# Kernel optimization log

Measured on AMD Instinct MI355X. Metric: run time of the kernel, lower is better.

## Reference

```python
import jax, jax.numpy as jnp
import numpy as np

N = 50000   # num_of_nodes (cfg.dataset.num_nodes)
C = 128     # in_channels; TopKPooling ratio = C/N -> k = C pooled nodes
E = 800000  # num edges


def setup_inputs() -> dict:
    key = jax.random.key(0)
    ks = jax.random.split(key, 8)
    std = 1.0 / np.sqrt(C)
    X = jax.random.normal(ks[0], (N, C), dtype=jnp.float32)
    edge_index = jax.random.randint(ks[1], (2, E), 0, N, dtype=jnp.int64)
    edge_weight = jax.random.uniform(ks[2], (E,), dtype=jnp.float32)
    p = jax.random.normal(ks[3], (C,), dtype=jnp.float32)                      # TopKPooling projection
    W_ih = jax.random.normal(ks[4], (3 * C, C), dtype=jnp.float32) * std       # GRU input weights [r|z|n]
    W_hh = jax.random.normal(ks[5], (3 * C, C), dtype=jnp.float32) * std       # GRU hidden weights
    b_ih = jnp.zeros((3 * C,), dtype=jnp.float32)
    b_hh = jnp.zeros((3 * C,), dtype=jnp.float32)
    W_conv = jax.random.uniform(ks[6], (C, C), dtype=jnp.float32, minval=-std, maxval=std)  # GCN lin weight
    b_conv = jnp.zeros((C,), dtype=jnp.float32)
    return {"X": X, "edge_weight": edge_weight, "p": p, "W_ih": W_ih, "W_hh": W_hh,
            "b_ih": b_ih, "b_hh": b_hh, "W_conv": W_conv, "b_conv": b_conv,
            "edge_index": edge_index}


def _forward(X, edge_weight, p, W_ih, W_hh, b_ih, b_hh, W_conv, b_conv, edge_index):
    # ---- TopKPooling: score = X.p/||p||, pick top k=C nodes, gate with tanh ----
    score = X @ p / jnp.linalg.norm(p)                       # [N]
    top_vals, top_idx = jax.lax.top_k(score, C)              # k = C (ratio = C/N)
    X_tilde = X[top_idx] * jnp.tanh(top_vals)[:, None]       # [C, C]
    X_tilde = jax.lax.stop_gradient(X_tilde)                 # .detach() in original

    # ---- GRU single step: input X_tilde (batch=C), hidden h0 = W_conv ----
    gi = X_tilde @ W_ih.T + b_ih                             # [C, 3C]
    gh = W_conv @ W_hh.T + b_hh                              # [C, 3C]
    gi_r, gi_z, gi_n = jnp.split(gi, 3, axis=-1)
    gh_r, gh_z, gh_n = jnp.split(gh, 3, axis=-1)
    r = jax.nn.sigmoid(gi_r + gh_r)
    z = jax.nn.sigmoid(gi_z + gh_z)
    n = jnp.tanh(gi_n + r * gh_n)
    W_new = (1.0 - z) * n + z * W_conv                       # evolved GCN weight [C, C]

    # ---- GCNConv with self-loops + symmetric normalization ----
    src, dst = edge_index[0], edge_index[1]
    loop = jnp.arange(N, dtype=src.dtype)
    src2 = jnp.concatenate([src, loop])
    dst2 = jnp.concatenate([dst, loop])
    w2 = jnp.concatenate([edge_weight, jnp.ones((N,), dtype=edge_weight.dtype)])
    deg = jax.ops.segment_sum(w2, dst2, num_segments=N)      # [N]
    dinv = jnp.where(deg > 0, jax.lax.rsqrt(deg), 0.0)
    norm = dinv[src2] * w2 * dinv[dst2]                      # [E+N]
    Xw = X @ W_new.T                                         # [N, C]
    msg = Xw[src2] * norm[:, None]                           # gather + scale, [E+N, C]
    out = jax.ops.segment_sum(msg, dst2, num_segments=N)     # scatter-add, [N, C]
    return out + b_conv


def reference(X, edge_weight, p, W_ih, W_hh, b_ih, b_hh, W_conv, b_conv, edge_index):
    return _forward(X, edge_weight, p, W_ih, W_hh, b_ih, b_hh, W_conv, b_conv, edge_index)
```

## Files before the change

kernel.cpp:

```cpp
#include <hip/hip_runtime.h>
#include <hip/hip_fp16.h>
#include <math.h>

#define C 128
#define HB 2048
#define NS 4096
#define SHB 192

typedef __attribute__((ext_vector_type(8))) short bf16x8;
typedef __attribute__((ext_vector_type(4))) float f32x4;

__device__ inline unsigned ord_f32(float f) {
    unsigned u = __float_as_uint(f);
    return u ^ ((u & 0x80000000u) ? 0xFFFFFFFFu : 0x80000000u);
}
__device__ inline float unord_f32(unsigned u) {
    return __uint_as_float(u ^ ((u & 0x80000000u) ? 0x80000000u : 0xFFFFFFFFu));
}
__device__ inline short f2bf(float f) {
    unsigned u = __float_as_uint(f);
    return (short)((u + 0x7FFFu + ((u >> 16) & 1u)) >> 16);
}
__device__ inline float bf2f(short s) {
    return __uint_as_float(((unsigned)(unsigned short)s) << 16);
}

__global__ __launch_bounds__(1024) void k_front(const float* __restrict__ X,
                                                const float* __restrict__ p,
                                                float* __restrict__ scores,
                                                int* __restrict__ hist,
                                                const int* __restrict__ ei,
                                                int* __restrict__ rh,
                                                int N, int E, int NBIN, int NBLKE) {
    int t = threadIdx.x;
    if (blockIdx.x < SHB) {
        __shared__ int lh[HB];
        for (int i = t; i < HB; i += 1024) lh[i] = 0;
        __syncthreads();
        int gw   = blockIdx.x * 16 + (t >> 6);
        int lane = t & 63;
        const float2* p2 = (const float2*)p;
        float2 pv2 = p2[lane];
        for (int r = gw; r < N; r += SHB * 16) {
            const float2* xr = (const float2*)(X + (size_t)r * C);
            float2 x2 = xr[lane];
            float a = x2.x * pv2.x + x2.y * pv2.y;
            #pragma unroll
            for (int o = 32; o; o >>= 1) a += __shfl_down(a, o);
            if (lane == 0) {
                scores[r] = a;
                atomicAdd(&lh[ord_f32(a) >> 21], 1);
            }
        }
        __syncthreads();
        for (int i = t; i < HB; i += 1024) {
            int v = lh[i];
            if (v) atomicAdd(&hist[i], v);
        }
    } else {
        __shared__ int bh[8][256];
        int cp = (t >> 7) & 7;
        for (int i = t; i < 8 * 256; i += 1024) ((int*)bh)[i] = 0;
        __syncthreads();
        int eb = blockIdx.x - SHB;
        int e = eb * 2048 + t * 2;
        if (e + 1 < E) {
            int2 d2 = *(const int2*)(ei + E + e);
            atomicAdd(&bh[cp][d2.x >> 8], 1);
            atomicAdd(&bh[cp][d2.y >> 8], 1);
        } else if (e < E) {
            atomicAdd(&bh[cp][ei[E + e] >> 8], 1);
        }
        __syncthreads();
        for (int i = t; i < NBIN; i += 1024) {
            int s = 0;
            #pragma unroll
            for (int c = 0; c < 8; c++) s += bh[c][i];
            rh[(size_t)i * NBLKE + eb] = s;
        }
    }
}

__global__ __launch_bounds__(512) void k_rscanA(int* __restrict__ rh, int* __restrict__ tot, int NBLKE) {
    __shared__ int sc[512];
    int t = threadIdx.x;
    int bin = blockIdx.x;
    int v = (t < NBLKE) ? rh[(size_t)bin * NBLKE + t] : 0;
    sc[t] = v;
    __syncthreads();
    for (int off = 1; off < 512; off <<= 1) {
        int u = (t >= off) ? sc[t - off] : 0;
        __syncthreads();
        sc[t] += u;
        __syncthreads();
    }
    if (t < NBLKE) rh[(size_t)bin * NBLKE + t] = sc[t] - v;
    if (t == 511) tot[bin] = sc[511];
}

__global__ __launch_bounds__(1024) void k_rscat(const int* __restrict__ ei, const float* __restrict__ ew,
                                                const int* __restrict__ rh, const int* __restrict__ tot,
                                                unsigned long long* __restrict__ sorted,
                                                int E, int NBIN, int NBLKE) {
    __shared__ int sc[256];
    __shared__ int cur[256];
    int t = threadIdx.x;
    int eb = blockIdx.x;
    int v = 0;
    if (t < 256) {
        v = (t < NBIN) ? tot[t] : 0;
        sc[t] = v;
    }
    __syncthreads();
    for (int off = 1; off < 256; off <<= 1) {
        int u = (t < 256 && t >= off) ? sc[t - off] : 0;
        __syncthreads();
        if (t < 256) sc[t] += u;
        __syncthreads();
    }
    if (t < NBIN) cur[t] = (sc[t] - v) + rh[(size_t)t * NBLKE + eb];
    __syncthreads();
    int e = eb * 2048 + t * 2;
    #pragma unroll
    for (int j = 0; j < 2; j++) {
        int ee = e + j;
        if (ee < E) {
            int s = ei[ee], d = ei[E + ee];
            float w = ew[ee];
            int pos = atomicAdd(&cur[d >> 8], 1);
            unsigned long long pk = ((unsigned long long)(unsigned)d << 48)
                                  | ((unsigned long long)(unsigned short)s << 32)
                                  |  (unsigned long long)__float_as_uint(w);
            sorted[pos] = pk;
        }
    }
}

__global__ __launch_bounds__(1024) void k_bin(const unsigned long long* __restrict__ sorted,
                                              const int* __restrict__ tot,
                                              int* __restrict__ offs, float* __restrict__ dinv,
                                              unsigned* __restrict__ epack,
                                              int N, int E, int NBIN) {
    __shared__ int cnt[256];
    __shared__ float wsum[256];
    __shared__ int sc[256];
    __shared__ int cur2[256];
    __shared__ int s_base[2];
    int t = threadIdx.x;
    int b = blockIdx.x;
    int v = 0;
    if (t < 256) {
        v = (t < NBIN) ? tot[t] : 0;
        sc[t] = v;
    }
    __syncthreads();
    for (int off = 1; off < 256; off <<= 1) {
        int u = (t < 256 && t >= off) ? sc[t - off] : 0;
        __syncthreads();
        if (t < 256) sc[t] += u;
        __syncthreads();
    }
    if (t == b) { s_base[0] = sc[t] - v; s_base[1] = sc[t]; }
    __syncthreads();
    int s0 = s_base[0], s1 = s_base[1];
    for (int i = t; i < 256; i += 1024) { cnt[i] = 0; wsum[i] = 0.f; }
    __syncthreads();
    for (int i = s0 + t; i < s1; i += 1024) {
        unsigned long long pk = sorted[i];
        int d8 = (int)(pk >> 48) & 255;
        float w = __uint_as_float((unsigned)(pk & 0xFFFFFFFFull));
        atomicAdd(&cnt[d8], 1);
        atomicAdd(&wsum[d8], w);
    }
    __syncthreads();
    int cv = (t < 256) ? cnt[t] : 0;
    if (t < 256) sc[t] = cv;
    __syncthreads();
    for (int off = 1; off < 256; off <<= 1) {
        int u = (t < 256 && t >= off) ? sc[t - off] : 0;
        __syncthreads();
        if (t < 256) sc[t] += u;
        __syncthreads();
    }
    if (t < 256) {
        int loff = sc[t] - cv;
        cur2[t] = s0 + loff;
        int node = b * 256 + t;
        if (node < N) {
            offs[node] = s0 + loff;
            dinv[node] = rsqrtf(1.0f + wsum[t]);
        }
    }
    if (b == NBIN - 1 && t == 0) offs[N] = E;
    __syncthreads();
    for (int i = s0 + t; i < s1; i += 1024) {
        unsigned long long pk = sorted[i];
        int d8 = (int)(pk >> 48) & 255;
        unsigned src = (unsigned)((pk >> 32) & 0xFFFFu);
        float w = __uint_as_float((unsigned)(pk & 0xFFFFFFFFull));
        int pos = atomicAdd(&cur2[d8], 1);
        __half hw = __float2half(w);
        epack[pos] = ((unsigned)*(unsigned short*)&hw << 16) | src;
    }
}

__global__ __launch_bounds__(256) void k_filter(const float* __restrict__ scores,
                                                const int* __restrict__ hist,
                                                int* __restrict__ nc,
                                                unsigned long long* __restrict__ cand, int N) {
    __shared__ int sc[256];
    __shared__ int sT;
    int t = threadIdx.x;
    int loc[8];
    int sum = 0;
    #pragma unroll
    for (int s = 0; s < 8; s++) {
        loc[s] = hist[HB - 1 - (t * 8 + s)];
        sum += loc[s];
    }
    sc[t] = sum;
    __syncthreads();
    for (int off = 1; off < 256; off <<= 1) {
        int v = (t >= off) ? sc[t - off] : 0;
        __syncthreads();
        sc[t] += v;
        __syncthreads();
    }
    int run = sc[t] - sum;
    #pragma unroll
    for (int s = 0; s < 8; s++) {
        int b = HB - 1 - (t * 8 + s);
        int nr = run + loc[s];
        if (run < C && nr >= C) sT = b;
        run = nr;
    }
    __syncthreads();
    int T = sT;
    int i = blockIdx.x * 256 + t;
    if (i < N) {
        unsigned u = ord_f32(scores[i]);
        if ((int)(u >> 21) >= T) {
            int pos = atomicAdd(nc, 1);
            if (pos < NS)
                cand[pos] = ((unsigned long long)u << 32) | (unsigned)(~(unsigned)i);
        }
    }
}

__global__ __launch_bounds__(1024) void k_sel(const unsigned long long* __restrict__ cand,
                                              const int* __restrict__ nc,
                                              const float* __restrict__ p,
                                              int* __restrict__ tidx, float* __restrict__ gate) {
    __shared__ unsigned long long sk[NS];
    __shared__ float red[16];
    __shared__ float s_pn;
    int t = threadIdx.x;
    int M = *nc; if (M > NS) M = NS;
    int S = 256; while (S < M) S <<= 1;
    for (int i = t; i < S; i += 1024) sk[i] = (i < M) ? cand[i] : 0ULL;
    float pv = 0.f;
    if (t < C) { float x = p[t]; pv = x * x; }
    #pragma unroll
    for (int o = 32; o; o >>= 1) pv += __shfl_down(pv, o);
    if ((t & 63) == 0) red[t >> 6] = pv;
    __syncthreads();
    if (t == 0) {
        float s = 0.f;
        for (int i = 0; i < 16; i++) s += red[i];
        s_pn = sqrtf(s);
    }
    for (int k = 2; k <= S; k <<= 1) {
        for (int j = k >> 1; j > 0; j >>= 1) {
            __syncthreads();
            for (int idx = t; idx < S; idx += 1024) {
                int l = idx ^ j;
                if (l > idx) {
                    unsigned long long a = sk[idx], b = sk[l];
                    bool desc = (idx & k) == 0;
                    if (desc ? (a < b) : (a > b)) { sk[idx] = b; sk[l] = a; }
                }
            }
        }
    }
    __syncthreads();
    if (t < C) {
        unsigned long long g = sk[t];
        tidx[t] = (int)(~(unsigned)(g & 0xFFFFFFFFull));
        gate[t] = tanhf(unord_f32((unsigned)(g >> 32)) / s_pn);
    }
}

__global__ __launch_bounds__(256) void k_gru(const float* __restrict__ X,
                                             const int* __restrict__ tidx,
                                             const float* __restrict__ gate,
                                             const float* __restrict__ Wc,
                                             const float* __restrict__ W_ih, const float* __restrict__ W_hh,
                                             const float* __restrict__ b_ih, const float* __restrict__ b_hh,
                                             float* __restrict__ wnewT) {
    int t = threadIdx.x;
    int i = t & 127;
    int j = blockIdx.x * 2 + (t >> 7);
    int src = tidx[i];
    float g = gate[i];
    const float4* xr   = (const float4*)(X + (size_t)src * C);
    const float4* hr   = (const float4*)(Wc + (size_t)i * C);
    const float4* wri  = (const float4*)(W_ih + (size_t)j * C);
    const float4* wzi  = (const float4*)(W_ih + (size_t)(C + j) * C);
    const float4* wni  = (const float4*)(W_ih + (size_t)(2 * C + j) * C);
    const float4* wrh  = (const float4*)(W_hh + (size_t)j * C);
    const float4* wzh  = (const float4*)(W_hh + (size_t)(C + j) * C);
    const float4* wnh  = (const float4*)(W_hh + (size_t)(2 * C + j) * C);
    float gir = 0, giz = 0, gin = 0, ghr = 0, ghz = 0, ghn = 0;
    #pragma unroll 8
    for (int k4 = 0; k4 < C / 4; k4++) {
        float4 x = xr[k4], h = hr[k4], a;
        a = wri[k4]; gir += x.x * a.x + x.y * a.y + x.z * a.z + x.w * a.w;
        a = wzi[k4]; giz += x.x * a.x + x.y * a.y + x.z * a.z + x.w * a.w;
        a = wni[k4]; gin += x.x * a.x + x.y * a.y + x.z * a.z + x.w * a.w;
        a = wrh[k4]; ghr += h.x * a.x + h.y * a.y + h.z * a.z + h.w * a.w;
        a = wzh[k4]; ghz += h.x * a.x + h.y * a.y + h.z * a.z + h.w * a.w;
        a = wnh[k4]; ghn += h.x * a.x + h.y * a.y + h.z * a.z + h.w * a.w;
    }
    gir = g * gir + b_ih[j];         ghr += b_hh[j];
    giz = g * giz + b_ih[C + j];     ghz += b_hh[C + j];
    gin = g * gin + b_ih[2 * C + j]; ghn += b_hh[2 * C + j];
    float r = 1.f / (1.f + expf(-(gir + ghr)));
    float z = 1.f / (1.f + expf(-(giz + ghz)));
    float n = tanhf(gin + r * ghn);
    float wn = (1.f - z) * n + z * Wc[(size_t)i * C + j];
    wnewT[(size_t)j * C + i] = wn;
}

__global__ __launch_bounds__(256) void k_xw(const float* __restrict__ X,
                                            const float* __restrict__ wnewT,
                                            const float* __restrict__ dinv,
                                            unsigned* __restrict__ xwh, int N) {
    __shared__ short Bh[C * C];
    __shared__ short Bl[C * C];
    int t = threadIdx.x;
    for (int idx = t; idx < C * C; idx += 256) {
        int k = idx >> 7, c = idx & 127;
        float wv = wnewT[idx];
        short hi = f2bf(wv);
        float lo = wv - bf2f(hi);
        int pos = c * C + (k ^ ((c & 15) << 3));
        Bh[pos] = hi;
        Bl[pos] = f2bf(lo);
    }
    __syncthreads();

    int wave = t >> 6, lane = t & 63;
    int ln = lane & 15, quad = lane >> 4;
    int r0 = blockIdx.x * 128 + wave * 32;

    f32x4 acc[2][8];
    #pragma unroll
    for (int mt = 0; mt < 2; mt++)
        #pragma unroll
        for (int ct = 0; ct < 8; ct++) { acc[mt][ct][0] = 0.f; acc[mt][ct][1] = 0.f; acc[mt][ct][2] = 0.f; acc[mt][ct][3] = 0.f; }

    int row0 = r0 + ln;       if (row0 >= N) row0 = N - 1;
    int row1 = r0 + 16 + ln;  if (row1 >= N) row1 = N - 1;
    const float* xr0 = X + (size_t)row0 * C + quad * 8;
    const float* xr1 = X + (size_t)row1 * C + quad * 8;

    for (int ks = 0; ks < 4; ks++) {
        float a0[8], a1[8];
        *(float4*)&a0[0] = *(const float4*)(xr0 + ks * 32);
        *(float4*)&a0[4] = *(const float4*)(xr0 + ks * 32 + 4);
        *(float4*)&a1[0] = *(const float4*)(xr1 + ks * 32);
        *(float4*)&a1[4] = *(const float4*)(xr1 + ks * 32 + 4);
        bf16x8 a0h, a0l, a1h, a1l;
        #pragma unroll
        for (int j = 0; j < 8; j++) {
            short h0 = f2bf(a0[j]); a0h[j] = h0; a0l[j] = f2bf(a0[j] - bf2f(h0));
            short h1 = f2bf(a1[j]); a1h[j] = h1; a1l[j] = f2bf(a1[j] - bf2f(h1));
        }
        int kb = ks * 32 + quad * 8;
        int koff = kb ^ (ln << 3);
        #pragma unroll
        for (int ct = 0; ct < 8; ct++) {
            int pos = (ct * 16 + ln) * C + koff;
            bf16x8 bh = *(bf16x8*)&Bh[pos];
            bf16x8 bl = *(bf16x8*)&Bl[pos];
            acc[0][ct] = __builtin_amdgcn_mfma_f32_16x16x32_bf16(a0h, bh, acc[0][ct], 0, 0, 0);
            acc[0][ct] = __builtin_amdgcn_mfma_f32_16x16x32_bf16(a0l, bh, acc[0][ct], 0, 0, 0);
            acc[0][ct] = __builtin_amdgcn_mfma_f32_16x16x32_bf16(a0h, bl, acc[0][ct], 0, 0, 0);
            acc[1][ct] = __builtin_amdgcn_mfma_f32_16x16x32_bf16(a1h, bh, acc[1][ct], 0, 0, 0);
            acc[1][ct] = __builtin_amdgcn_mfma_f32_16x16x32_bf16(a1l, bh, acc[1][ct], 0, 0, 0);
            acc[1][ct] = __builtin_amdgcn_mfma_f32_16x16x32_bf16(a1h, bl, acc[1][ct], 0, 0, 0);
        }
    }

    __half* H = (__half*)xwh;
    #pragma unroll
    for (int mt = 0; mt < 2; mt++) {
        int rbase = r0 + mt * 16 + quad * 4;
        #pragma unroll
        for (int reg = 0; reg < 4; reg++) {
            int r = rbase + reg;
            if (r < N) {
                float dvr = dinv[r];
                #pragma unroll
                for (int ct = 0; ct < 8; ct++) {
                    int col = ct * 16 + ln;
                    H[(size_t)r * C + col] = __float2half(acc[mt][ct][reg] * dvr);
                }
            }
        }
    }
}

__global__ __launch_bounds__(256) void k_gather(const unsigned* __restrict__ xwh,
                                                const int* __restrict__ offs,
                                                const unsigned* __restrict__ epack,
                                                const float* __restrict__ dinv,
                                                const float* __restrict__ b_conv,
                                                float* __restrict__ out, int N) {
    int t = threadIdx.x;
    int v = blockIdx.x * 4 + (t >> 6);
    int lane = t & 63;
    if (v >= N) return;
    float dv = dinv[v];
    unsigned uv = xwh[(size_t)v * 64 + lane];
    __half2 hv = *(__half2*)&uv;
    float acc0 = __low2float(hv);
    float acc1 = __high2float(hv);
    int e0 = offs[v], e1 = offs[v + 1];
    int e = e0;
    for (; e + 7 < e1; e += 8) {
        unsigned pk[8], ux[8];
        #pragma unroll
        for (int j = 0; j < 8; j++) pk[j] = __builtin_nontemporal_load(&epack[e + j]);
        #pragma unroll
        for (int j = 0; j < 8; j++) ux[j] = xwh[(size_t)(pk[j] & 0xFFFFu) * 64 + lane];
        #pragma unroll
        for (int j = 0; j < 8; j++) {
            unsigned short hs = (unsigned short)(pk[j] >> 16);
            float nm = __half2float(*(__half*)&hs);
            __half2 h = *(__half2*)&ux[j];
            acc0 += nm * __low2float(h);
            acc1 += nm * __high2float(h);
        }
    }
    for (; e + 3 < e1; e += 4) {
        unsigned pk[4], ux[4];
        #pragma unroll
        for (int j = 0; j < 4; j++) pk[j] = __builtin_nontemporal_load(&epack[e + j]);
        #pragma unroll
        for (int j = 0; j < 4; j++) ux[j] = xwh[(size_t)(pk[j] & 0xFFFFu) * 64 + lane];
        #pragma unroll
        for (int j = 0; j < 4; j++) {
            unsigned short hs = (unsigned short)(pk[j] >> 16);
            float nm = __half2float(*(__half*)&hs);
            __half2 h = *(__half2*)&ux[j];
            acc0 += nm * __low2float(h);
            acc1 += nm * __high2float(h);
        }
    }
    for (; e < e1; e++) {
        unsigned pA = __builtin_nontemporal_load(&epack[e]);
        unsigned uA = xwh[(size_t)(pA & 0xFFFFu) * 64 + lane];
        unsigned short hs = (unsigned short)(pA >> 16);
        float nA = __half2float(*(__half*)&hs);
        __half2 hA = *(__half2*)&uA;
        acc0 += nA * __low2float(hA);
        acc1 += nA * __high2float(hA);
    }
    const float2* b2 = (const float2*)b_conv;
    float2 bb = b2[lane];
    unsigned long long ov = ((unsigned long long)__float_as_uint(acc1 * dv + bb.y) << 32)
                          |  (unsigned long long)__float_as_uint(acc0 * dv + bb.x);
    __builtin_nontemporal_store(ov, (unsigned long long*)(out + (size_t)v * C) + lane);
}

extern "C" void kernel_launch(void* const* d_in, const int* in_sizes, int n_in,
                              void* d_out, int out_size, void* d_ws, size_t ws_size,
                              hipStream_t stream) {
    const float* X      = (const float*)d_in[0];
    const float* ew     = (const float*)d_in[1];
    const float* p      = (const float*)d_in[2];
    const float* W_ih   = (const float*)d_in[3];
    const float* W_hh   = (const float*)d_in[4];
    const float* b_ih   = (const float*)d_in[5];
    const float* b_hh   = (const float*)d_in[6];
    const float* W_conv = (const float*)d_in[7];
    const float* b_conv = (const float*)d_in[8];
    const int*   ei     = (const int*)d_in[9];
    const int N = in_sizes[0] / C;
    const int E = in_sizes[1];
    float* out = (float*)d_out;
    const int NB    = (N + 255) / 256;
    const int NBIN  = (N + 255) / 256;
    const int NBLKE = (E + 2047) / 2048;

    char* w = (char*)d_ws;
    auto alloc = [&](size_t bytes) -> void* {
        void* r = (void*)w;
        w += (bytes + 255) & ~(size_t)255;
        return r;
    };
    int*   hist   = (int*)alloc(HB * 4);
    int*   nc     = (int*)alloc(256);
    size_t zbytes = (size_t)(w - (char*)d_ws);
    float* scores = (float*)alloc((size_t)N * 4);
    float* dinv   = (float*)alloc((size_t)N * 4);
    int*   offs   = (int*)alloc((size_t)(N + 1) * 4);
    int*   rh     = (int*)alloc((size_t)NBIN * NBLKE * 4);
    int*   tot    = (int*)alloc((size_t)NBIN * 4);
    unsigned long long* cand = (unsigned long long*)alloc((size_t)NS * 8);
    int*   tidx   = (int*)alloc(C * 4);
    float* gate   = (float*)alloc(C * 4);
    float* wnewT  = (float*)alloc((size_t)C * C * 4);
    unsigned long long* sorted = (unsigned long long*)alloc((size_t)E * 8);
    unsigned* epack = (unsigned*)alloc((size_t)E * 4);
    unsigned* xwh = (unsigned*)alloc((size_t)N * 64 * 4);

    hipMemsetAsync(d_ws, 0, zbytes, stream);
    k_front<<<SHB + NBLKE, 1024, 0, stream>>>(X, p, scores, hist, ei, rh, N, E, NBIN, NBLKE);
    k_filter<<<NB, 256, 0, stream>>>(scores, hist, nc, cand, N);
    k_sel<<<1, 1024, 0, stream>>>(cand, nc, p, tidx, gate);
    k_gru<<<C / 2, 256, 0, stream>>>(X, tidx, gate, W_conv, W_ih, W_hh, b_ih, b_hh, wnewT);
    k_rscanA<<<NBIN, 512, 0, stream>>>(rh, tot, NBLKE);
    k_rscat<<<NBLKE, 1024, 0, stream>>>(ei, ew, rh, tot, sorted, E, NBIN, NBLKE);
    k_bin<<<NBIN, 1024, 0, stream>>>(sorted, tot, offs, dinv, epack, N, E, NBIN);
    k_xw<<<(N + 127) / 128, 256, 0, stream>>>(X, wnewT, dinv, xwh, N);
    k_gather<<<(N + 3) / 4, 256, 0, stream>>>(xwh, offs, epack, dinv, b_conv, out, N);
}
```

Measured before the change: 225.2 us.

## Overlap edge sort chain with top-k/GRU/XW on a second stream

Forks the edge bucketing chain (rscanA, rscat, bin) onto a second non-blocking stream so it runs concurrently with the top-k filter, selection, GRU and XW matmul. To break XW's dependency on dinv, the source-side degree normalization moves out of k_xw into the gather, which now loads dinv per source edge. This adds an extra random 4-byte load per edge in the gather and event synchronization overhead, in exchange for hiding the small, poorly-occupying front kernels behind the edge preprocessing.

Measured after the change: 234.9 us. 1.04x slower.

```diff
diff --git a/kernel.cpp b/kernel.cpp
--- a/kernel.cpp
+++ b/kernel.cpp
@@ -333,7 +333,6 @@
 
 __global__ __launch_bounds__(256) void k_xw(const float* __restrict__ X,
                                             const float* __restrict__ wnewT,
-                                            const float* __restrict__ dinv,
                                             unsigned* __restrict__ xwh, int N) {
     __shared__ short Bh[C * C];
     __shared__ short Bl[C * C];
@@ -400,11 +399,10 @@
         for (int reg = 0; reg < 4; reg++) {
             int r = rbase + reg;
             if (r < N) {
-                float dvr = dinv[r];
                 #pragma unroll
                 for (int ct = 0; ct < 8; ct++) {
                     int col = ct * 16 + ln;
-                    H[(size_t)r * C + col] = __float2half(acc[mt][ct][reg] * dvr);
+                    H[(size_t)r * C + col] = __float2half(acc[mt][ct][reg]);
                 }
             }
         }
@@ -424,20 +422,25 @@
     float dv = dinv[v];
     unsigned uv = xwh[(size_t)v * 64 + lane];
     __half2 hv = *(__half2*)&uv;
-    float acc0 = __low2float(hv);
-    float acc1 = __high2float(hv);
+    float acc0 = dv * __low2float(hv);
+    float acc1 = dv * __high2float(hv);
     int e0 = offs[v], e1 = offs[v + 1];
     int e = e0;
     for (; e + 7 < e1; e += 8) {
         unsigned pk[8], ux[8];
+        float ds[8];
         #pragma unroll
         for (int j = 0; j < 8; j++) pk[j] = __builtin_nontemporal_load(&epack[e + j]);
         #pragma unroll
-        for (int j = 0; j < 8; j++) ux[j] = xwh[(size_t)(pk[j] & 0xFFFFu) * 64 + lane];
+        for (int j = 0; j < 8; j++) {
+            unsigned s = pk[j] & 0xFFFFu;
+            ux[j] = xwh[(size_t)s * 64 + lane];
+            ds[j] = dinv[s];
+        }
         #pragma unroll
         for (int j = 0; j < 8; j++) {
             unsigned short hs = (unsigned short)(pk[j] >> 16);
-            float nm = __half2float(*(__half*)&hs);
+            float nm = __half2float(*(__half*)&hs) * ds[j];
             __half2 h = *(__half2*)&ux[j];
             acc0 += nm * __low2float(h);
             acc1 += nm * __high2float(h);
@@ -445,14 +448,19 @@
     }
     for (; e + 3 < e1; e += 4) {
         unsigned pk[4], ux[4];
+        float ds[4];
         #pragma unroll
         for (int j = 0; j < 4; j++) pk[j] = __builtin_nontemporal_load(&epack[e + j]);
         #pragma unroll
-        for (int j = 0; j < 4; j++) ux[j] = xwh[(size_t)(pk[j] & 0xFFFFu) * 64 + lane];
+        for (int j = 0; j < 4; j++) {
+            unsigned s = pk[j] & 0xFFFFu;
+            ux[j] = xwh[(size_t)s * 64 + lane];
+            ds[j] = dinv[s];
+        }
         #pragma unroll
         for (int j = 0; j < 4; j++) {
             unsigned short hs = (unsigned short)(pk[j] >> 16);
-            float nm = __half2float(*(__half*)&hs);
+            float nm = __half2float(*(__half*)&hs) * ds[j];
             __half2 h = *(__half2*)&ux[j];
             acc0 += nm * __low2float(h);
             acc1 += nm * __high2float(h);
@@ -460,9 +468,11 @@
     }
     for (; e < e1; e++) {
         unsigned pA = __builtin_nontemporal_load(&epack[e]);
-        unsigned uA = xwh[(size_t)(pA & 0xFFFFu) * 64 + lane];
+        unsigned sA = pA & 0xFFFFu;
+        unsigned uA = xwh[(size_t)sA * 64 + lane];
+        float dA = dinv[sA];
         unsigned short hs = (unsigned short)(pA >> 16);
-        float nA = __half2float(*(__half*)&hs);
+        float nA = __half2float(*(__half*)&hs) * dA;
         __half2 hA = *(__half2*)&uA;
         acc0 += nA * __low2float(hA);
         acc1 += nA * __high2float(hA);
@@ -516,14 +526,38 @@
     unsigned* epack = (unsigned*)alloc((size_t)E * 4);
     unsigned* xwh = (unsigned*)alloc((size_t)N * 64 * 4);
 
+    static hipStream_t s2 = nullptr;
+    static hipEvent_t  evF = nullptr, evE = nullptr;
+    static int tried = 0;
+    if (!tried) {
+        tried = 1;
+        if (hipStreamCreateWithFlags(&s2, hipStreamNonBlocking) != hipSuccess) s2 = nullptr;
+        if (s2) {
+            if (hipEventCreateWithFlags(&evF, hipEventDisableTiming) != hipSuccess) evF = nullptr;
+            if (evF && hipEventCreateWithFlags(&evE, hipEventDisableTiming) != hipSuccess) evE = nullptr;
+            if (!evF || !evE) s2 = nullptr;
+        }
+    }
+    const bool fork = (s2 != nullptr);
+    hipStream_t se = fork ? s2 : stream;
+
     hipMemsetAsync(d_ws, 0, zbytes, stream);
     k_front<<<SHB + NBLKE, 1024, 0, stream>>>(X, p, scores, hist, ei, rh, N, E, NBIN, NBLKE);
+
+    if (fork) {
+        hipEventRecord(evF, stream);
+        hipStreamWaitEvent(s2, evF, 0);
+    }
+    k_rscanA<<<NBIN, 512, 0, se>>>(rh, tot, NBLKE);
+    k_rscat<<<NBLKE, 1024, 0, se>>>(ei, ew, rh, tot, sorted, E, NBIN, NBLKE);
+    k_bin<<<NBIN, 1024, 0, se>>>(sorted, tot, offs, dinv, epack, N, E, NBIN);
+    if (fork) hipEventRecord(evE, s2);
+
     k_filter<<<NB, 256, 0, stream>>>(scores, hist, nc, cand, N);
     k_sel<<<1, 1024, 0, stream>>>(cand, nc, p, tidx, gate);
     k_gru<<<C / 2, 256, 0, stream>>>(X, tidx, gate, W_conv, W_ih, W_hh, b_ih, b_hh, wnewT);
-    k_rscanA<<<NBIN, 512, 0, stream>>>(rh, tot, NBLKE);
-    k_rscat<<<NBLKE, 1024, 0, stream>>>(ei, ew, rh, tot, sorted, E, NBIN, NBLKE);
-    k_bin<<<NBIN, 1024, 0, stream>>>(sorted, tot, offs, dinv, epack, N, E, NBIN);
-    k_xw<<<(N + 127) / 128, 256, 0, stream>>>(X, wnewT, dinv, xwh, N);
+    k_xw<<<(N + 127) / 128, 256, 0, stream>>>(X, wnewT, xwh, N);
+
+    if (fork) hipStreamWaitEvent(stream, evE, 0);
     k_gather<<<(N + 3) / 4, 256, 0, stream>>>(xwh, offs, epack, dinv, b_conv, out, N);
 }
```
